# Kernel optimization log

Measured on AMD Instinct MI355X. Metric: run time of the kernel, lower is better.

The kernel has to match this reference:

```python
import jax, jax.numpy as jnp
import numpy as np

N_ATOMS = 131072
NUM_GS = 128
HIDDEN = 512
N_MOL = 1024


def setup_inputs() -> dict:
    key = jax.random.key(0)
    ks = jax.random.split(key, 16)
    Gs = jax.random.normal(ks[0], (N_ATOMS, NUM_GS), dtype=jnp.float32)
    types = jax.random.randint(ks[1], (N_ATOMS,), 0, 2, dtype=jnp.int32)
    mol_id = jnp.sort(jax.random.randint(ks[2], (N_ATOMS,), 0, N_MOL, dtype=jnp.int32))

    def dense(k, fi, fo):
        return (jax.random.normal(k, (fi, fo), dtype=jnp.float32) / np.float32(np.sqrt(fi)))

    params = {}
    for i, t in enumerate(("A", "B")):
        base = 3 + i * 3
        params[f"W1_{t}"] = dense(ks[base], NUM_GS, HIDDEN)
        params[f"b1_{t}"] = jnp.zeros((HIDDEN,), jnp.float32)
        params[f"W2_{t}"] = dense(ks[base + 1], HIDDEN, HIDDEN)
        params[f"b2_{t}"] = jnp.zeros((HIDDEN,), jnp.float32)
        params[f"W3_{t}"] = dense(ks[base + 2], HIDDEN, 1)
        params[f"b3_{t}"] = jnp.zeros((1,), jnp.float32)
        params[f"off_{t}"] = jnp.zeros((1,), jnp.float32)
    return {"Gs": Gs, "types": types, "mol_id": mol_id, **params}


def _ann(G, W1, b1, W2, b2, W3, b3, off):
    # Atomic NN: two tanh hidden layers, linear scalar output + trainable offset
    h = jnp.tanh(G @ W1 + b1)
    h = jnp.tanh(h @ W2 + b2)
    return (h @ W3 + b3 + off)[:, 0]  # [N]


def reference(Gs, types, mol_id,
              W1_A, b1_A, W2_A, b2_A, W3_A, b3_A, off_A,
              W1_B, b1_B, W2_B, b2_B, W3_B, b3_B, off_B):
    # Per-type expert MLPs; dense-select is the math-equivalent of
    # dynamic_partition -> per-type ANN -> dynamic_stitch for 2 experts.
    eA = _ann(Gs, W1_A, b1_A, W2_A, b2_A, W3_A, b3_A, off_A)
    eB = _ann(Gs, W1_B, b1_B, W2_B, b2_B, W3_B, b3_B, off_B)
    atom_e = jnp.where(types == 0, eA, eB)  # [N_ATOMS]
    # Ragged per-molecule reduce_sum == segment_sum over sorted mol ids
    mol_e = jax.ops.segment_sum(atom_e, mol_id, num_segments=N_MOL)
    counts = jax.ops.segment_sum(jnp.ones_like(atom_e), mol_id, num_segments=N_MOL)
    energy_per_atom = mol_e / jnp.maximum(counts, 1.0)
    return energy_per_atom[:, None]  # [N_MOL, 1]
```

## Files before the change

### kernel.cpp

```cpp
#include <hip/hip_runtime.h>

typedef _Float16 half8  __attribute__((ext_vector_type(8)));
typedef _Float16 half4v __attribute__((ext_vector_type(4)));
typedef __fp16   fp16x2 __attribute__((ext_vector_type(2)));
typedef float    floatx4 __attribute__((ext_vector_type(4)));

#define N_ATOMS 131072
#define NUM_GS  128
#define HIDDEN  512
#define N_MOL   1024

#define BM      32
#define NB_SIDE (N_ATOMS / BM)
#define NT_TOT  (HIDDEN / 16)
#define SH1_LD  (HIDDEN + 8)

#define WS_CNT_OFF     0
#define WS_MOLSUM_OFF  1024
#define WS_PERM_OFF    9216
#define WS_W1FA_OFF    533504
#define WS_W1FB_OFF    664576
#define WS_W2FA_OFF    795648
#define WS_W2FB_OFF    1319936
#define WS_ZERO_BYTES  5120

__device__ __forceinline__ float fast_tanh(float x) {
    float e = exp2f(x * 2.8853900817779268f);
    float r = __builtin_amdgcn_rcpf(e + 1.0f);
    return fmaf(-2.0f, r, 1.0f);
}

__global__ __launch_bounds__(256)
void prep_kernel(const int* __restrict__ types,
                 const float* __restrict__ W1A, const float* __restrict__ W1B,
                 const float* __restrict__ W2A, const float* __restrict__ W2B,
                 int* __restrict__ cnt, int* __restrict__ perm,
                 _Float16* __restrict__ W1FA, _Float16* __restrict__ W1FB,
                 _Float16* __restrict__ W2FA, _Float16* __restrict__ W2FB) {
    __shared__ float tile[32][65];
    const int p   = blockIdx.x;
    const int tid = threadIdx.x;

    if (p < 512) {
        __shared__ int sCA[4];
        __shared__ int sBaseA, sBaseB;
        const int i    = p * 256 + tid;
        const int lane = tid & 63;
        const int w    = tid >> 6;
        const bool isA = (types[i] == 0);
        unsigned long long mask = __ballot(isA);
        unsigned long long lt   = ((unsigned long long)1 << lane) - 1;
        int rA = __popcll(mask & lt);
        if (lane == 0) sCA[w] = __popcll(mask);
        __syncthreads();
        if (tid == 0) {
            int tot = sCA[0] + sCA[1] + sCA[2] + sCA[3];
            sBaseA = atomicAdd(&cnt[0], tot);
            sBaseB = atomicAdd(&cnt[1], 256 - tot);
        }
        __syncthreads();
        int preA = 0;
        #pragma unroll
        for (int k = 0; k < 4; ++k) preA += (k < w) ? sCA[k] : 0;
        int preB = w * 64 - preA;
        int rB   = lane - rA;
        if (isA) perm[sBaseA + preA + rA] = i;
        else     perm[N_ATOMS - 1 - (sBaseB + preB + rB)] = i;
        return;
    }

    const float* src; _Float16* dst; int pb;
    if (p < 544)      { src = W1A; dst = W1FA; pb = p - 512; }
    else if (p < 576) { src = W1B; dst = W1FB; pb = p - 544; }
    else if (p < 704) { src = W2A; dst = W2FA; pb = p - 576; }
    else              { src = W2B; dst = W2FB; pb = p - 704; }
    const int bx = pb & 7;
    const int by = pb >> 3;
    const int n0 = bx * 64, k0 = by * 32;
    #pragma unroll
    for (int i = 0; i < 8; ++i) {
        int idx = tid + i * 256;
        int r = idx >> 6, c = idx & 63;
        tile[r][c] = src[(size_t)(k0 + r) * HIDDEN + n0 + c];
    }
    __syncthreads();
    const int nt_l = tid >> 6, lane = tid & 63;
    const int l15 = lane & 15, q = lane >> 4;
    half8 v;
    #pragma unroll
    for (int j = 0; j < 8; ++j)
        v[j] = (_Float16)tile[q * 8 + j][nt_l * 16 + l15];
    const int ntile = bx * 4 + nt_l;
    *(half8*)(dst + (((size_t)by * NT_TOT + ntile) * 64 + lane) * 8) = v;
}

__global__ __launch_bounds__(256, 3)
void mlp_kernel(const float* __restrict__ Gs,
                const int*   __restrict__ mol_id,
                const _Float16* __restrict__ W1FA, const _Float16* __restrict__ W2FA,
                const float* __restrict__ b1A, const float* __restrict__ b2A,
                const float* __restrict__ W3A, const float* __restrict__ b3A,
                const float* __restrict__ offA,
                const _Float16* __restrict__ W1FB, const _Float16* __restrict__ W2FB,
                const float* __restrict__ b1B, const float* __restrict__ b2B,
                const float* __restrict__ W3B, const float* __restrict__ b3B,
                const float* __restrict__ offB,
                const int* __restrict__ cnt, const int* __restrict__ perm,
                float* __restrict__ mol_sum) {
    __shared__ __align__(16) _Float16 sGh[BM][NUM_GS + 8];
    __shared__ __align__(16) _Float16 sH1[BM][SH1_LD];
    __shared__ int   sOrig[BM];
    __shared__ float sPart[4][BM];

    const int b     = blockIdx.x;
    const int nA    = cnt[0];
    const int sideB = (b >= NB_SIDE) ? 1 : 0;
    const int r0    = (sideB ? b - NB_SIDE : b) * BM;
    const int nSide = sideB ? (N_ATOMS - nA) : nA;
    if (r0 >= nSide) return;

    const _Float16 *W1F, *W2F;
    const float *b1, *b2, *W3;
    float b3off;
    if (!sideB) { W1F = W1FA; W2F = W2FA; b1 = b1A; b2 = b2A; W3 = W3A; b3off = b3A[0] + offA[0]; }
    else        { W1F = W1FB; W2F = W2FB; b1 = b1B; b2 = b2B; W3 = W3B; b3off = b3B[0] + offB[0]; }

    const int tid = threadIdx.x;
    if (tid < BM) {
        int r = r0 + tid;
        int orig = -1;
        if (r < nSide) orig = sideB ? perm[N_ATOMS - 1 - r] : perm[r];
        sOrig[tid] = orig;
    }
    __syncthreads();

    #pragma unroll
    for (int i = 0; i < 4; ++i) {
        int idx = tid + 256 * i;
        int row = idx >> 5;
        int c4  = idx & 31;
        int orig = sOrig[row];
        float4 v = make_float4(0.f, 0.f, 0.f, 0.f);
        if (orig >= 0) v = ((const float4*)(Gs + (size_t)orig * NUM_GS))[c4];
        union { half4v h4; fp16x2 h2[2]; } hu;
        hu.h2[0] = __builtin_amdgcn_cvt_pkrtz(v.x, v.y);
        hu.h2[1] = __builtin_amdgcn_cvt_pkrtz(v.z, v.w);
        *(half4v*)&sGh[row][c4 * 4] = hu.h4;
    }
    __syncthreads();

    const int lane = tid & 63;
    const int wid  = tid >> 6;
    const int l15  = lane & 15;
    const int quad = lane >> 4;

    floatx4 acc[2][8];
    #pragma unroll
    for (int mt = 0; mt < 2; ++mt)
        #pragma unroll
        for (int nt = 0; nt < 8; ++nt) acc[mt][nt] = (floatx4){0.f, 0.f, 0.f, 0.f};

    #pragma unroll
    for (int ks = 0; ks < NUM_GS / 32; ++ks) {
        half8 a0 = *(const half8*)&sGh[l15][ks * 32 + quad * 8];
        half8 a1 = *(const half8*)&sGh[l15 + 16][ks * 32 + quad * 8];
        #pragma unroll
        for (int nt = 0; nt < 8; ++nt) {
            int ntile = wid * 8 + nt;
            half8 bf = *(const half8*)(W1F + (((size_t)ks * NT_TOT + ntile) * 64 + lane) * 8);
            acc[0][nt] = __builtin_amdgcn_mfma_f32_16x16x32_f16(a0, bf, acc[0][nt], 0, 0, 0);
            acc[1][nt] = __builtin_amdgcn_mfma_f32_16x16x32_f16(a1, bf, acc[1][nt], 0, 0, 0);
        }
    }
    #pragma unroll
    for (int nt = 0; nt < 8; ++nt) {
        int col = wid * 128 + nt * 16 + l15;
        float b1v = b1[col];
        #pragma unroll
        for (int mt = 0; mt < 2; ++mt)
            #pragma unroll
            for (int r = 0; r < 4; ++r)
                sH1[mt * 16 + quad * 4 + r][col] = (_Float16)fast_tanh(acc[mt][nt][r] + b1v);
    }
    __syncthreads();

    #pragma unroll
    for (int mt = 0; mt < 2; ++mt)
        #pragma unroll
        for (int nt = 0; nt < 8; ++nt) acc[mt][nt] = (floatx4){0.f, 0.f, 0.f, 0.f};

    #pragma unroll 4
    for (int ks = 0; ks < HIDDEN / 32; ++ks) {
        half8 a0 = *(const half8*)&sH1[l15][ks * 32 + quad * 8];
        half8 a1 = *(const half8*)&sH1[l15 + 16][ks * 32 + quad * 8];
        #pragma unroll
        for (int nt = 0; nt < 8; ++nt) {
            int ntile = wid * 8 + nt;
            half8 bf = *(const half8*)(W2F + (((size_t)ks * NT_TOT + ntile) * 64 + lane) * 8);
            acc[0][nt] = __builtin_amdgcn_mfma_f32_16x16x32_f16(a0, bf, acc[0][nt], 0, 0, 0);
            acc[1][nt] = __builtin_amdgcn_mfma_f32_16x16x32_f16(a1, bf, acc[1][nt], 0, 0, 0);
        }
    }

    float p[2][4];
    #pragma unroll
    for (int mt = 0; mt < 2; ++mt)
        #pragma unroll
        for (int r = 0; r < 4; ++r) p[mt][r] = 0.f;

    #pragma unroll
    for (int nt = 0; nt < 8; ++nt) {
        int col = wid * 128 + nt * 16 + l15;
        float b2v = b2[col];
        float w3v = W3[col];
        #pragma unroll
        for (int mt = 0; mt < 2; ++mt)
            #pragma unroll
            for (int r = 0; r < 4; ++r) {
                float t = fast_tanh(acc[mt][nt][r] + b2v);
                p[mt][r] = fmaf(t, w3v, p[mt][r]);
            }
    }
    #pragma unroll
    for (int mt = 0; mt < 2; ++mt)
        #pragma unroll
        for (int r = 0; r < 4; ++r) {
            float v = p[mt][r];
            v += __shfl_xor(v, 1, 64);
            v += __shfl_xor(v, 2, 64);
            v += __shfl_xor(v, 4, 64);
            v += __shfl_xor(v, 8, 64);
            p[mt][r] = v;
        }
    if (l15 == 0) {
        #pragma unroll
        for (int mt = 0; mt < 2; ++mt)
            #pragma unroll
            for (int r = 0; r < 4; ++r)
                sPart[wid][mt * 16 + quad * 4 + r] = p[mt][r];
    }
    __syncthreads();
    if (tid < BM) {
        int orig = sOrig[tid];
        if (orig >= 0) {
            float e = sPart[0][tid] + sPart[1][tid] + sPart[2][tid] + sPart[3][tid] + b3off;
            atomicAdd(&mol_sum[mol_id[orig]], e);
        }
    }
}

__global__ void finalize_kernel(const float* __restrict__ mol_sum,
                                const int* __restrict__ mol_id,
                                float* __restrict__ out) {
    int m = blockIdx.x * blockDim.x + threadIdx.x;
    if (m >= N_MOL) return;
    int lo0 = 0, hi0 = N_ATOMS;
    while (lo0 < hi0) { int mid = (lo0 + hi0) >> 1; if (mol_id[mid] < m) lo0 = mid + 1; else hi0 = mid; }
    int lo1 = lo0, hi1 = N_ATOMS;
    while (lo1 < hi1) { int mid = (lo1 + hi1) >> 1; if (mol_id[mid] < m + 1) lo1 = mid + 1; else hi1 = mid; }
    float c = (float)(lo1 - lo0);
    out[m] = mol_sum[m] / fmaxf(c, 1.0f);
}

extern "C" void kernel_launch(void* const* d_in, const int* in_sizes, int n_in,
                              void* d_out, int out_size, void* d_ws, size_t ws_size,
                              hipStream_t stream) {
    const float* Gs     = (const float*)d_in[0];
    const int*   types  = (const int*)d_in[1];
    const int*   mol_id = (const int*)d_in[2];
    const float* W1A = (const float*)d_in[3];
    const float* b1A = (const float*)d_in[4];
    const float* W2A = (const float*)d_in[5];
    const float* b2A = (const float*)d_in[6];
    const float* W3A = (const float*)d_in[7];
    const float* b3A = (const float*)d_in[8];
    const float* oA  = (const float*)d_in[9];
    const float* W1B = (const float*)d_in[10];
    const float* b1B = (const float*)d_in[11];
    const float* W2B = (const float*)d_in[12];
    const float* b2B = (const float*)d_in[13];
    const float* W3B = (const float*)d_in[14];
    const float* b3B = (const float*)d_in[15];
    const float* oB  = (const float*)d_in[16];

    char* ws = (char*)d_ws;
    int*      cnt     = (int*)(ws + WS_CNT_OFF);
    float*    mol_sum = (float*)(ws + WS_MOLSUM_OFF);
    int*      perm    = (int*)(ws + WS_PERM_OFF);
    _Float16* W1FA    = (_Float16*)(ws + WS_W1FA_OFF);
    _Float16* W1FB    = (_Float16*)(ws + WS_W1FB_OFF);
    _Float16* W2FA    = (_Float16*)(ws + WS_W2FA_OFF);
    _Float16* W2FB    = (_Float16*)(ws + WS_W2FB_OFF);
    float* out = (float*)d_out;

    hipMemsetAsync(d_ws, 0, WS_ZERO_BYTES, stream);
    prep_kernel<<<832, 256, 0, stream>>>(types, W1A, W1B, W2A, W2B,
                                         cnt, perm,
                                         W1FA, W1FB, W2FA, W2FB);
    mlp_kernel<<<2 * NB_SIDE, 256, 0, stream>>>(
        Gs, mol_id,
        W1FA, W2FA, b1A, b2A, W3A, b3A, oA,
        W1FB, W2FB, b1B, b2B, W3B, b3B, oB,
        cnt, perm, mol_sum);
    finalize_kernel<<<(N_MOL + 255) / 256, 256, 0, stream>>>(mol_sum, mol_id, out);
}
```

Baseline: 291.7 us.

## Double row tile to 64 atoms with 8 waves and alias LDS buffers

The MLP kernel now handles 64 atoms per block with 512 threads (8 waves). Each wave computes a 4x4 grid of MFMA tiles over 64 columns instead of 2x8 over 128, so each fp16 weight fragment loaded from global memory is reused across four row tiles instead of two, roughly halving weight traffic per atom. The Gs staging buffer and the first hidden-layer buffer now share one LDS allocation, with an extra barrier before it is overwritten, to keep shared memory per block small. The risks are fewer blocks in flight, more idle rows in the last partial tile of each type, and the added synchronisation.

```diff
diff --git a/kernel.cpp b/kernel.cpp
--- a/kernel.cpp
+++ b/kernel.cpp
@@ -10,10 +10,11 @@
 #define HIDDEN  512
 #define N_MOL   1024
 
-#define BM      32
+#define BM      64
 #define NB_SIDE (N_ATOMS / BM)
 #define NT_TOT  (HIDDEN / 16)
 #define SH1_LD  (HIDDEN + 8)
+#define SGH_LD  (NUM_GS + 8)
 
 #define WS_CNT_OFF     0
 #define WS_MOLSUM_OFF  1024
@@ -94,7 +95,7 @@
     *(half8*)(dst + (((size_t)by * NT_TOT + ntile) * 64 + lane) * 8) = v;
 }
 
-__global__ __launch_bounds__(256, 3)
+__global__ __launch_bounds__(512, 4)
 void mlp_kernel(const float* __restrict__ Gs,
                 const int*   __restrict__ mol_id,
                 const _Float16* __restrict__ W1FA, const _Float16* __restrict__ W2FA,
@@ -107,10 +108,12 @@
                 const float* __restrict__ offB,
                 const int* __restrict__ cnt, const int* __restrict__ perm,
                 float* __restrict__ mol_sum) {
-    __shared__ __align__(16) _Float16 sGh[BM][NUM_GS + 8];
-    __shared__ __align__(16) _Float16 sH1[BM][SH1_LD];
+    __shared__ __align__(16) _Float16 sBuf[BM * SH1_LD];
     __shared__ int   sOrig[BM];
-    __shared__ float sPart[4][BM];
+    __shared__ float sPart[8][BM];
+
+    _Float16 (*sH1)[SH1_LD] = (_Float16(*)[SH1_LD])sBuf;
+    _Float16 (*sGh)[SGH_LD] = (_Float16(*)[SGH_LD])sBuf;
 
     const int b     = blockIdx.x;
     const int nA    = cnt[0];
@@ -136,7 +139,7 @@
 
     #pragma unroll
     for (int i = 0; i < 4; ++i) {
-        int idx = tid + 256 * i;
+        int idx = tid + 512 * i;
         int row = idx >> 5;
         int c4  = idx & 31;
         int orig = sOrig[row];
@@ -154,30 +157,35 @@
     const int l15  = lane & 15;
     const int quad = lane >> 4;
 
-    floatx4 acc[2][8];
-    #pragma unroll
-    for (int mt = 0; mt < 2; ++mt)
-        #pragma unroll
-        for (int nt = 0; nt < 8; ++nt) acc[mt][nt] = (floatx4){0.f, 0.f, 0.f, 0.f};
+    floatx4 acc[4][4];
+    #pragma unroll
+    for (int mt = 0; mt < 4; ++mt)
+        #pragma unroll
+        for (int nt = 0; nt < 4; ++nt) acc[mt][nt] = (floatx4){0.f, 0.f, 0.f, 0.f};
 
     #pragma unroll
     for (int ks = 0; ks < NUM_GS / 32; ++ks) {
-        half8 a0 = *(const half8*)&sGh[l15][ks * 32 + quad * 8];
-        half8 a1 = *(const half8*)&sGh[l15 + 16][ks * 32 + quad * 8];
-        #pragma unroll
-        for (int nt = 0; nt < 8; ++nt) {
-            int ntile = wid * 8 + nt;
+        half8 a[4];
+        #pragma unroll
+        for (int mt = 0; mt < 4; ++mt)
+            a[mt] = *(const half8*)&sGh[mt * 16 + l15][ks * 32 + quad * 8];
+        #pragma unroll
+        for (int nt = 0; nt < 4; ++nt) {
+            int ntile = wid * 4 + nt;
             half8 bf = *(const half8*)(W1F + (((size_t)ks * NT_TOT + ntile) * 64 + lane) * 8);
-            acc[0][nt] = __builtin_amdgcn_mfma_f32_16x16x32_f16(a0, bf, acc[0][nt], 0, 0, 0);
-            acc[1][nt] = __builtin_amdgcn_mfma_f32_16x16x32_f16(a1, bf, acc[1][nt], 0, 0, 0);
-        }
-    }
-    #pragma unroll
-    for (int nt = 0; nt < 8; ++nt) {
-        int col = wid * 128 + nt * 16 + l15;
+            #pragma unroll
+            for (int mt = 0; mt < 4; ++mt)
+                acc[mt][nt] = __builtin_amdgcn_mfma_f32_16x16x32_f16(a[mt], bf, acc[mt][nt], 0, 0, 0);
+        }
+    }
+    __syncthreads();
+
+    #pragma unroll
+    for (int nt = 0; nt < 4; ++nt) {
+        int col = wid * 64 + nt * 16 + l15;
         float b1v = b1[col];
         #pragma unroll
-        for (int mt = 0; mt < 2; ++mt)
+        for (int mt = 0; mt < 4; ++mt)
             #pragma unroll
             for (int r = 0; r < 4; ++r)
                 sH1[mt * 16 + quad * 4 + r][col] = (_Float16)fast_tanh(acc[mt][nt][r] + b1v);
@@ -185,36 +193,39 @@
     __syncthreads();
 
     #pragma unroll
-    for (int mt = 0; mt < 2; ++mt)
-        #pragma unroll
-        for (int nt = 0; nt < 8; ++nt) acc[mt][nt] = (floatx4){0.f, 0.f, 0.f, 0.f};
+    for (int mt = 0; mt < 4; ++mt)
+        #pragma unroll
+        for (int nt = 0; nt < 4; ++nt) acc[mt][nt] = (floatx4){0.f, 0.f, 0.f, 0.f};
 
     #pragma unroll 4
     for (int ks = 0; ks < HIDDEN / 32; ++ks) {
-        half8 a0 = *(const half8*)&sH1[l15][ks * 32 + quad * 8];
-        half8 a1 = *(const half8*)&sH1[l15 + 16][ks * 32 + quad * 8];
-        #pragma unroll
-        for (int nt = 0; nt < 8; ++nt) {
-            int ntile = wid * 8 + nt;
+        half8 a[4];
+        #pragma unroll
+        for (int mt = 0; mt < 4; ++mt)
+            a[mt] = *(const half8*)&sH1[mt * 16 + l15][ks * 32 + quad * 8];
+        #pragma unroll
+        for (int nt = 0; nt < 4; ++nt) {
+            int ntile = wid * 4 + nt;
             half8 bf = *(const half8*)(W2F + (((size_t)ks * NT_TOT + ntile) * 64 + lane) * 8);
-            acc[0][nt] = __builtin_amdgcn_mfma_f32_16x16x32_f16(a0, bf, acc[0][nt], 0, 0, 0);
-            acc[1][nt] = __builtin_amdgcn_mfma_f32_16x16x32_f16(a1, bf, acc[1][nt], 0, 0, 0);
-        }
-    }
-
-    float p[2][4];
-    #pragma unroll
-    for (int mt = 0; mt < 2; ++mt)
+            #pragma unroll
+            for (int mt = 0; mt < 4; ++mt)
+                acc[mt][nt] = __builtin_amdgcn_mfma_f32_16x16x32_f16(a[mt], bf, acc[mt][nt], 0, 0, 0);
+        }
+    }
+
+    float p[4][4];
+    #pragma unroll
+    for (int mt = 0; mt < 4; ++mt)
         #pragma unroll
         for (int r = 0; r < 4; ++r) p[mt][r] = 0.f;
 
     #pragma unroll
-    for (int nt = 0; nt < 8; ++nt) {
-        int col = wid * 128 + nt * 16 + l15;
+    for (int nt = 0; nt < 4; ++nt) {
+        int col = wid * 64 + nt * 16 + l15;
         float b2v = b2[col];
         float w3v = W3[col];
         #pragma unroll
-        for (int mt = 0; mt < 2; ++mt)
+        for (int mt = 0; mt < 4; ++mt)
             #pragma unroll
             for (int r = 0; r < 4; ++r) {
                 float t = fast_tanh(acc[mt][nt][r] + b2v);
@@ -222,7 +233,7 @@
             }
     }
     #pragma unroll
-    for (int mt = 0; mt < 2; ++mt)
+    for (int mt = 0; mt < 4; ++mt)
         #pragma unroll
         for (int r = 0; r < 4; ++r) {
             float v = p[mt][r];
@@ -234,7 +245,7 @@
         }
     if (l15 == 0) {
         #pragma unroll
-        for (int mt = 0; mt < 2; ++mt)
+        for (int mt = 0; mt < 4; ++mt)
             #pragma unroll
             for (int r = 0; r < 4; ++r)
                 sPart[wid][mt * 16 + quad * 4 + r] = p[mt][r];
@@ -243,7 +254,9 @@
     if (tid < BM) {
         int orig = sOrig[tid];
         if (orig >= 0) {
-            float e = sPart[0][tid] + sPart[1][tid] + sPart[2][tid] + sPart[3][tid] + b3off;
+            float e = b3off;
+            #pragma unroll
+            for (int w = 0; w < 8; ++w) e += sPart[w][tid];
             atomicAdd(&mol_sum[mol_id[orig]], e);
         }
     }
@@ -297,7 +310,7 @@
     prep_kernel<<<832, 256, 0, stream>>>(types, W1A, W1B, W2A, W2B,
                                          cnt, perm,
                                          W1FA, W1FB, W2FA, W2FB);
-    mlp_kernel<<<2 * NB_SIDE, 256, 0, stream>>>(
+    mlp_kernel<<<2 * NB_SIDE, 512, 0, stream>>>(
         Gs, mol_id,
         W1FA, W2FA, b1A, b2A, W3A, b3A, oA,
         W1FB, W2FB, b1B, b2B, W3B, b3B, oB,
```

New measurement: 307.0 us. +5.3%, slower.
